# Kernel tuning notes

Measured on AMD Instinct MI355X. Metric: run time of the kernel, lower is better.

Reference implementation:

```python
import jax, jax.numpy as jnp
import numpy as np

# dims
B, N = 8, 64            # graphs, nodes per graph (equal-size ragged batch)
IN_DIM, EDGE_DIM = 16, 8
D, H = 128, 4
DH = D // H             # 32
L = 3                   # num_layers
FF = 4 * D              # 512
OUT = 1
SCALE = float(np.sqrt(DH))


def setup_inputs() -> dict:
    key = jax.random.key(0)
    ks = jax.random.split(key, 24)
    w = lambda k, s: jax.random.normal(k, s, jnp.float32) * 0.02
    return {
        'x': jax.random.normal(ks[0], (B, N, IN_DIM), jnp.float32),
        'edge_attr': jax.random.normal(ks[1], (B, N, N, EDGE_DIM), jnp.float32),
        'edge_mask': jax.random.bernoulli(ks[2], 0.2, (B, N, N)),
        # feature encoder (linear node + linear edge encoders, learned no-edge token)
        'node_W': w(ks[3], (IN_DIM, D)), 'node_b': jnp.zeros((D,), jnp.float32),
        'edge_W': w(ks[4], (EDGE_DIM, D)), 'edge_b': jnp.zeros((D,), jnp.float32),
        'no_edge': w(ks[5], (D,)),
        # per-layer edge-transformer params (stacked over L for lax.scan)
        'Wq': w(ks[6], (L, D, D)), 'Wk': w(ks[7], (L, D, D)),
        'Wv1': w(ks[8], (L, D, D)), 'Wv2': w(ks[9], (L, D, D)),
        'Wo': w(ks[10], (L, D, D)), 'bo': jnp.zeros((L, D), jnp.float32),
        'ln1_g': jnp.ones((L, D), jnp.float32), 'ln1_b': jnp.zeros((L, D), jnp.float32),
        'W1': w(ks[11], (L, D, FF)), 'b1': jnp.zeros((L, FF), jnp.float32),
        'W2': w(ks[12], (L, FF, D)), 'b2': jnp.zeros((L, D), jnp.float32),
        'ln2_g': jnp.ones((L, D), jnp.float32), 'ln2_b': jnp.zeros((L, D), jnp.float32),
        'Wout': w(ks[13], (D, OUT)), 'bout': jnp.zeros((OUT,), jnp.float32),
    }


def _ln(t, g, b):
    m = t.mean(-1, keepdims=True)
    v = t.var(-1, keepdims=True)
    return (t - m) * jax.lax.rsqrt(v + 1e-5) * g + b


def _forward(x, edge_attr, edge_mask, node_W, node_b, edge_W, edge_b, no_edge,
             Wq, Wk, Wv1, Wv2, Wo, bo, ln1_g, ln1_b, W1, b1, W2, b2,
             ln2_g, ln2_b, Wout, bout):
    # feature encoding: pair-token grid [B,N,N,D]
    node_emb = x @ node_W + node_b                       # [B,N,D]
    edge_emb = edge_attr @ edge_W + edge_b               # [B,N,N,D]
    tok = jnp.where(edge_mask[..., None], edge_emb, no_edge)
    eye = jnp.eye(N, dtype=bool)
    tok = jnp.where(eye[None, :, :, None], node_emb[:, :, None, :], tok)

    def heads(t, W):
        return (t @ W).reshape(B, N, N, H, DH)

    def layer(tok, p):
        wq, wk, wv1, wv2, wo, bo_, g1, b1_, w1, bf1, w2, bf2, g2, b2_ = p
        q = heads(tok, wq); k = heads(tok, wk)
        v1 = heads(tok, wv1); v2 = heads(tok, wv2)
        # triangular attention: token (i,j) attends over intermediate l
        s = jnp.einsum('bilhd,bljhd->bhilj', q, k) / SCALE   # [B,H,N,N,N]
        a = jax.nn.softmax(s, axis=3)                        # softmax over l
        o = jnp.einsum('bhilj,bilhd,bljhd->bijhd', a, v1, v2).reshape(B, N, N, D)
        tok = _ln(tok + o @ wo + bo_, g1, b1_)
        f = jax.nn.relu(tok @ w1 + bf1) @ w2 + bf2
        tok = _ln(tok + f, g2, b2_)
        return tok, None

    tok, _ = jax.lax.scan(
        layer, tok,
        (Wq, Wk, Wv1, Wv2, Wo, bo, ln1_g, ln1_b, W1, b1, W2, b2, ln2_g, ln2_b))

    diag = tok[:, jnp.arange(N), jnp.arange(N), :]           # node tokens [B,N,D]
    return diag @ Wout + bout                                 # [B,N,OUT]


def reference(x, edge_attr, edge_mask, node_W, node_b, edge_W, edge_b, no_edge,
              Wq, Wk, Wv1, Wv2, Wo, bo, ln1_g, ln1_b, W1, b1, W2, b2,
              ln2_g, ln2_b, Wout, bout):
    return _forward(x, edge_attr, edge_mask, node_W, node_b, edge_W, edge_b,
                    no_edge, Wq, Wk, Wv1, Wv2, Wo, bo, ln1_g, ln1_b,
                    W1, b1, W2, b2, ln2_g, ln2_b, Wout, bout)
```

## Files before the change

kernel.cpp:

```cpp
#include <hip/hip_runtime.h>

typedef unsigned short u16;
typedef __attribute__((ext_vector_type(8))) short bf16x8;
typedef __attribute__((ext_vector_type(4))) float f32x4;

#define INV_SCALE 0.17677669529663687f

static __device__ __forceinline__ float b2f(u16 u) {
    union { unsigned int i; float f; } v; v.i = ((unsigned int)u) << 16; return v.f;
}
static __device__ __forceinline__ u16 f2b(float f) {
    union { float f; unsigned int i; } v; v.f = f;
    unsigned int r = (v.i + 0x7FFFu + ((v.i >> 16) & 1u)) >> 16;
    return (u16)r;
}

#define NSEG 23
__device__ __constant__ int d_seg_off[NSEG + 1] = {
    0, 8192, 270336, 272384, 272512, 273536, 273664, 273792, 322944, 372096,
    421248, 470400, 519552, 519936, 520320, 520704, 717312, 718848, 915456,
    915840, 916224, 916608, 916736, 916744};
static const int h_seg_off[NSEG + 1] = {
    0, 8192, 270336, 272384, 272512, 273536, 273664, 273792, 322944, 372096,
    421248, 470400, 519552, 519936, 520320, 520704, 717312, 718848, 915456,
    915840, 916224, 916608, 916736, 916744};
#define ARENA_TOTAL 916744

struct ParamPtrs { const void* p[NSEG]; };

__global__ __launch_bounds__(256) void convert_params(ParamPtrs pp, u16* __restrict__ arena,
                                                      const void* __restrict__ mask,
                                                      int* __restrict__ mode) {
    if (blockIdx.x == 0) {
        __shared__ int f16, f32s, u8s;
        int tid = threadIdx.x;
        if (tid == 0) { f16 = 0; f32s = 0; u8s = 0; }
        __syncthreads();
        const u16* mu = (const u16*)mask;
        const unsigned int* mw = (const unsigned int*)mask;
        if (mu[2 * tid] == 0x3F80u) atomicOr(&f16, 1);
        if (mw[tid] == 0x3F800000u) atomicOr(&f32s, 1);
        if (mw[tid] > 1u) atomicOr(&u8s, 1);
        __syncthreads();
        if (tid == 0) mode[0] = f16 ? 0 : (f32s ? 3 : (u8s ? 1 : 2));
    }
    const unsigned int probe = ((const unsigned int*)pp.p[13])[0];
    const bool f32 = (probe == 0x3F800000u);
    for (int e = blockIdx.x * 256 + threadIdx.x; e < ARENA_TOTAL; e += gridDim.x * 256) {
        int k = 0;
        #pragma unroll
        for (int s2 = 1; s2 < NSEG; ++s2) if (e >= d_seg_off[s2]) k = s2;
        int local = e - d_seg_off[k];
        int src = local;
        if (k >= 7 && k <= 11) {
            int l = local >> 14, rem = local & 16383;
            int n = rem >> 7, kk = rem & 127;
            src = (l << 14) + kk * 128 + n;
        } else if (k == 15) {
            int l = local >> 16, rem = local & 65535;
            int n = rem >> 7, kk = rem & 127;
            src = (l << 16) + kk * 512 + n;
        } else if (k == 17) {
            int l = local >> 16, rem = local & 65535;
            int n = rem >> 9, kk = rem & 511;
            src = (l << 16) + kk * 128 + n;
        }
        u16 v;
        if (k == 22 && local >= 1) v = 0;
        else v = f32 ? f2b(((const float*)pp.p[k])[src]) : ((const u16*)pp.p[k])[src];
        arena[e] = v;
    }
}

__global__ __launch_bounds__(256) void assemble_kernel(
    const u16* __restrict__ x, const u16* __restrict__ ea,
    const void* __restrict__ mask, const int* __restrict__ modeptr,
    const u16* __restrict__ nodeW, const u16* __restrict__ nodeB,
    const u16* __restrict__ edgeW, const u16* __restrict__ edgeB, const u16* __restrict__ noedge,
    float* __restrict__ tokf, u16* __restrict__ tokb)
{
    const int md = modeptr[0];
    int g = blockIdx.x * 256 + threadIdx.x;
    int t = g >> 5, dq = g & 31, d0 = dq * 4;
    int b = t >> 12, i = (t >> 6) & 63, j = t & 63;
    float v[4];
    if (i == j) {
        #pragma unroll
        for (int c = 0; c < 4; c++) v[c] = b2f(nodeB[d0 + c]);
        #pragma unroll
        for (int e = 0; e < 16; e++) {
            float xe = b2f(x[(b * 64 + i) * 16 + e]);
            #pragma unroll
            for (int c = 0; c < 4; c++) v[c] += xe * b2f(nodeW[e * 128 + d0 + c]);
        }
    } else {
        bool edge;
        if (md == 0)      edge = ((const u16*)mask)[t] != 0;
        else if (md == 3) edge = ((const float*)mask)[t] != 0.0f;
        else if (md == 1) edge = ((const unsigned char*)mask)[t] != 0;
        else              edge = ((const unsigned int*)mask)[t] != 0;
        if (edge) {
            #pragma unroll
            for (int c = 0; c < 4; c++) v[c] = b2f(edgeB[d0 + c]);
            #pragma unroll
            for (int e = 0; e < 8; e++) {
                float ae = b2f(ea[t * 8 + e]);
                #pragma unroll
                for (int c = 0; c < 4; c++) v[c] += ae * b2f(edgeW[e * 128 + d0 + c]);
            }
        } else {
            #pragma unroll
            for (int c = 0; c < 4; c++) v[c] = b2f(noedge[d0 + c]);
        }
    }
    *(float4*)(tokf + (size_t)t * 128 + d0) = make_float4(v[0], v[1], v[2], v[3]);
    u16 pk[4];
    #pragma unroll
    for (int c = 0; c < 4; c++) pk[c] = f2b(v[c]);
    *(uint2*)(tokb + (size_t)t * 128 + d0) = *(uint2*)pk;
}

__global__ __launch_bounds__(256) void gemm_qkv_kernel(
    const u16* __restrict__ A,
    const u16* __restrict__ B0, const u16* __restrict__ B1,
    const u16* __restrict__ B2, const u16* __restrict__ B3,
    float* __restrict__ v1f,
    u16* __restrict__ qb, u16* __restrict__ kb, u16* __restrict__ v2b)
{
    __shared__ __align__(16) u16 smem[2 * 128 * 72];
    u16* As = smem;
    u16* Bs = smem + 128 * 72;
    int tid = threadIdx.x;
    int m0 = blockIdx.x * 128;
    int by = blockIdx.y;
    const u16* Bp = (by == 0) ? B0 : (by == 1) ? B1 : (by == 2) ? B2 : B3;

    int w = tid >> 6, lane = tid & 63;
    int q = lane >> 4, r16 = lane & 15;
    int rw = (w >> 1) * 64, cw = (w & 1) * 64;

    f32x4 acc[4][4];
    #pragma unroll
    for (int mi = 0; mi < 4; mi++)
        #pragma unroll
        for (int ni = 0; ni < 4; ni++) acc[mi][ni] = (f32x4){0.f, 0.f, 0.f, 0.f};

    #pragma unroll
    for (int kt = 0; kt < 2; ++kt) {
        int k0 = kt * 64;
        __syncthreads();
        #pragma unroll
        for (int it = 0; it < 4; ++it) {
            int idx = tid + it * 256;
            int row = idx >> 3, ch = idx & 7;
            uint4 d = *(const uint4*)(A + (size_t)(m0 + row) * 128 + k0 + ch * 8);
            *(uint4*)&As[row * 72 + ch * 8] = d;
        }
        #pragma unroll
        for (int it = 0; it < 4; ++it) {
            int idx = tid + it * 256;
            int n = idx >> 3, ch = idx & 7;
            uint4 d = *(const uint4*)(Bp + (size_t)n * 128 + k0 + ch * 8);
            int ch2 = ch ^ ((n >> 3) & 7);
            *(uint4*)&Bs[n * 72 + ch2 * 8] = d;
        }
        __syncthreads();
        #pragma unroll
        for (int ks = 0; ks < 2; ++ks) {
            bf16x8 fa[4], fb[4];
            #pragma unroll
            for (int mi = 0; mi < 4; mi++)
                fa[mi] = *(const bf16x8*)&As[(rw + mi * 16 + r16) * 72 + ks * 32 + q * 8];
            #pragma unroll
            for (int ni = 0; ni < 4; ni++) {
                int n = cw + ni * 16 + r16;
                int ch2 = (ks * 4 + q) ^ ((n >> 3) & 7);
                fb[ni] = *(const bf16x8*)&Bs[n * 72 + ch2 * 8];
            }
            #pragma unroll
            for (int mi = 0; mi < 4; mi++)
                #pragma unroll
                for (int ni = 0; ni < 4; ni++)
                    acc[mi][ni] = __builtin_amdgcn_mfma_f32_16x16x32_bf16(fa[mi], fb[ni], acc[mi][ni], 0, 0, 0);
        }
    }

    int bl = m0 >> 12, it0 = (m0 >> 6) & 63;
    __syncthreads();
    if (by == 2) {
        float* cf = (float*)smem;
        #pragma unroll
        for (int hp = 0; hp < 2; ++hp) {
            if (hp) __syncthreads();
            if ((cw >> 6) == hp) {
                #pragma unroll
                for (int mi = 0; mi < 4; mi++) {
                    #pragma unroll
                    for (int ni = 0; ni < 4; ni++) {
                        int colh = (cw & 63) + ni * 16 + r16;
                        int ch4 = colh >> 2, cl = colh & 3;
                        #pragma unroll
                        for (int rr = 0; rr < 4; rr++) {
                            int r = rw + mi * 16 + q * 4 + rr;
                            cf[r * 64 + (((ch4 ^ (r & 15)) << 2) | cl)] = acc[mi][ni][rr];
                        }
                    }
                }
            }
            __syncthreads();
            #pragma unroll
            for (int it = 0; it < 8; ++it) {
                int idx = tid + it * 256;
                int hh = idx >> 10, itl = (idx >> 9) & 1, jt = (idx >> 3) & 63, d4 = idx & 7;
                int r = itl * 64 + jt;
                int colh = hh * 32 + d4 * 4;
                f32x4 v = *(const f32x4*)&cf[r * 64 + (((colh >> 2) ^ (r & 15)) << 2)];
                int h = hp * 2 + hh;
                *(f32x4*)&v1f[((((size_t)(bl * 4 + h)) * 64 + it0 + itl) * 64 + jt) * 32 + d4 * 4] = v;
            }
        }
    } else {
        u16* cs = smem;
        #pragma unroll
        for (int mi = 0; mi < 4; mi++) {
            #pragma unroll
            for (int ni = 0; ni < 4; ni++) {
                int col = cw + ni * 16 + r16;
                int ch = col >> 3, cl = col & 7;
                #pragma unroll
                for (int rr = 0; rr < 4; rr++) {
                    int r = rw + mi * 16 + q * 4 + rr;
                    cs[r * 128 + (((ch ^ (r & 15)) << 3) | cl)] = f2b(acc[mi][ni][rr]);
                }
            }
        }
        __syncthreads();
        if (by == 0) {
            #pragma unroll
            for (int it = 0; it < 8; ++it) {
                int idx = tid + it * 256;
                int h = idx >> 9, jt = (idx >> 3) & 63, itl = (idx >> 2) & 1, d8 = idx & 3;
                int r = itl * 64 + jt, c8 = h * 4 + d8;
                uint4 d = *(const uint4*)&cs[r * 128 + ((c8 ^ (r & 15)) << 3)];
                *(uint4*)&qb[((((size_t)(bl * 4 + h)) * 64 + jt) * 64 + it0 + itl) * 32 + d8 * 8] = d;
            }
        } else {
            u16* dp = (by == 1) ? kb : v2b;
            #pragma unroll
            for (int it = 0; it < 8; ++it) {
                int idx = tid + it * 256;
                int h = idx >> 9, itl = (idx >> 8) & 1, jt = (idx >> 2) & 63, d8 = idx & 3;
                int r = itl * 64 + jt, c8 = h * 4 + d8;
                uint4 d = *(const uint4*)&cs[r * 128 + ((c8 ^ (r & 15)) << 3)];
                *(uint4*)&dp[((((size_t)(bl * 4 + h)) * 64 + it0 + itl) * 64 + jt) * 32 + d8 * 8] = d;
            }
        }
    }
}

__global__ __launch_bounds__(256) void gemm_ln_kernel(
    const u16* __restrict__ A,
    const u16* __restrict__ BT,
    const u16* __restrict__ bias,
    float* __restrict__ tokf,
    const u16* __restrict__ lng, const u16* __restrict__ lnb, u16* __restrict__ tokbO)
{
    __shared__ __align__(16) u16 smem[64 * 72 + 128 * 72];
    u16* As = smem;
    u16* Bs = smem + 64 * 72;
    int tid = threadIdx.x;
    int m0 = blockIdx.x * 64;
    int w = tid >> 6, lane = tid & 63;
    int q = lane >> 4, r16 = lane & 15;
    int rw = (w >> 1) * 32, cw = (w & 1) * 64;

    f32x4 acc[2][4];
    #pragma unroll
    for (int mi = 0; mi < 2; mi++)
        #pragma unroll
        for (int ni = 0; ni < 4; ni++) acc[mi][ni] = (f32x4){0.f, 0.f, 0.f, 0.f};

    #pragma unroll
    for (int kt = 0; kt < 2; ++kt) {
        int k0 = kt * 64;
        __syncthreads();
        #pragma unroll
        for (int it = 0; it < 2; ++it) {
            int idx = tid + it * 256;
            int row = idx >> 3, ch = idx & 7;
            uint4 d = *(const uint4*)(A + (size_t)(m0 + row) * 128 + k0 + ch * 8);
            *(uint4*)&As[row * 72 + ch * 8] = d;
        }
        #pragma unroll
        for (int it = 0; it < 4; ++it) {
            int idx = tid + it * 256;
            int n = idx >> 3, ch = idx & 7;
            uint4 d = *(const uint4*)(BT + (size_t)n * 128 + k0 + ch * 8);
            int ch2 = ch ^ ((n >> 3) & 7);
            *(uint4*)&Bs[n * 72 + ch2 * 8] = d;
        }
        __syncthreads();
        #pragma unroll
        for (int ks = 0; ks < 2; ++ks) {
            bf16x8 fa[2], fb[4];
            #pragma unroll
            for (int mi = 0; mi < 2; mi++)
                fa[mi] = *(const bf16x8*)&As[(rw + mi * 16 + r16) * 72 + ks * 32 + q * 8];
            #pragma unroll
            for (int ni = 0; ni < 4; ni++) {
                int n = cw + ni * 16 + r16;
                int ch2 = (ks * 4 + q) ^ ((n >> 3) & 7);
                fb[ni] = *(const bf16x8*)&Bs[n * 72 + ch2 * 8];
            }
            #pragma unroll
            for (int mi = 0; mi < 2; mi++)
                #pragma unroll
                for (int ni = 0; ni < 4; ni++)
                    acc[mi][ni] = __builtin_amdgcn_mfma_f32_16x16x32_bf16(fa[mi], fb[ni], acc[mi][ni], 0, 0, 0);
        }
    }

    __syncthreads();
    float* cf  = (float*)smem;
    float* rsm = cf + 64 * 64;
    float* rqm = rsm + 128;
    int half = cw >> 6;
    #pragma unroll
    for (int ni = 0; ni < 4; ni++) {
        int col = cw + ni * 16 + r16;
        float bb = b2f(bias[col]);
        #pragma unroll
        for (int mi = 0; mi < 2; mi++)
            #pragma unroll
            for (int rr = 0; rr < 4; rr++) {
                int r = rw + mi * 16 + q * 4 + rr;
                acc[mi][ni][rr] += bb + tokf[(size_t)(m0 + r) * 128 + col];
            }
    }
    #pragma unroll
    for (int mi = 0; mi < 2; mi++)
        #pragma unroll
        for (int rr = 0; rr < 4; rr++) {
            float s = 0.f, sq = 0.f;
            #pragma unroll
            for (int ni = 0; ni < 4; ni++) { float t = acc[mi][ni][rr]; s += t; sq += t * t; }
            #pragma unroll
            for (int off = 1; off < 16; off <<= 1) {
                s  += __shfl_xor(s,  off, 16);
                sq += __shfl_xor(sq, off, 16);
            }
            if (r16 == 0) {
                int r = rw + mi * 16 + q * 4 + rr;
                rsm[half * 64 + r] = s;
                rqm[half * 64 + r] = sq;
            }
        }
    __syncthreads();
    float gl[4], bv[4];
    #pragma unroll
    for (int ni = 0; ni < 4; ni++) {
        int col = cw + ni * 16 + r16;
        gl[ni] = b2f(lng[col]);
        bv[ni] = b2f(lnb[col]);
    }
    #pragma unroll
    for (int mi = 0; mi < 2; mi++)
        #pragma unroll
        for (int rr = 0; rr < 4; rr++) {
            int r = rw + mi * 16 + q * 4 + rr;
            float tot = rsm[r] + rsm[64 + r];
            float tq  = rqm[r] + rqm[64 + r];
            float mean = tot * 0.0078125f;
            float var  = tq * 0.0078125f - mean * mean;
            float rstd = rsqrtf(var + 1e-5f);
            #pragma unroll
            for (int ni = 0; ni < 4; ni++)
                acc[mi][ni][rr] = (acc[mi][ni][rr] - mean) * rstd * gl[ni] + bv[ni];
        }
    #pragma unroll
    for (int hp = 0; hp < 2; ++hp) {
        __syncthreads();
        if (half == hp) {
            #pragma unroll
            for (int mi = 0; mi < 2; mi++)
                #pragma unroll
                for (int ni = 0; ni < 4; ni++) {
                    int colh = (cw & 63) + ni * 16 + r16;
                    int ch4 = colh >> 2, cl = colh & 3;
                    #pragma unroll
                    for (int rr = 0; rr < 4; rr++) {
                        int r = rw + mi * 16 + q * 4 + rr;
                        cf[r * 64 + (((ch4 ^ (r & 15)) << 2) | cl)] = acc[mi][ni][rr];
                    }
                }
        }
        __syncthreads();
        #pragma unroll
        for (int it = 0; it < 4; ++it) {
            int idx = tid + it * 256;
            int r = idx >> 4, c4 = idx & 15;
            f32x4 v = *(const f32x4*)&cf[r * 64 + ((c4 ^ (r & 15)) << 2)];
            int col = hp * 64 + c4 * 4;
            *(f32x4*)(tokf + (size_t)(m0 + r) * 128 + col) = v;
            u16 pk[4];
            #pragma unroll
            for (int e = 0; e < 4; e++) pk[e] = f2b(v[e]);
            *(uint2*)(tokbO + (size_t)(m0 + r) * 128 + col) = *(uint2*)pk;
        }
    }
}

__global__ __launch_bounds__(256) void ff_kernel(
    const u16* __restrict__ A,
    const u16* __restrict__ W1T, const u16* __restrict__ b1,
    const u16* __restrict__ W2T, const u16* __restrict__ b2,
    const u16* __restrict__ lng, const u16* __restrict__ lnb,
    float* __restrict__ tokf, u16* __restrict__ tokbO)
{
    __shared__ __align__(16) u16 smem[64 * 72 + 128 * 72];
    u16* As = smem;
    u16* Bs = smem + 64 * 72;
    int tid = threadIdx.x;
    int m0 = blockIdx.x * 64;
    int w = tid >> 6, lane = tid & 63;
    int q = lane >> 4, r16 = lane & 15;
    int rw = (w >> 1) * 32, cw = (w & 1) * 64;

    f32x4 acc2[2][4];
    #pragma unroll
    for (int mi = 0; mi < 2; mi++)
        #pragma unroll
        for (int ni = 0; ni < 4; ni++) acc2[mi][ni] = (f32x4){0.f, 0.f, 0.f, 0.f};

    for (int hs = 0; hs < 4; ++hs) {
        f32x4 acc1[2][4];
        #pragma unroll
        for (int mi = 0; mi < 2; mi++)
            #pragma unroll
            for (int ni = 0; ni < 4; ni++) acc1[mi][ni] = (f32x4){0.f, 0.f, 0.f, 0.f};
        #pragma unroll
        for (int kt = 0; kt < 2; ++kt) {
            int k0 = kt * 64;
            __syncthreads();
            #pragma unroll
            for (int it = 0; it < 2; ++it) {
                int idx = tid + it * 256;
                int row = idx >> 3, ch = idx & 7;
                uint4 d = *(const uint4*)(A + (size_t)(m0 + row) * 128 + k0 + ch * 8);
                *(uint4*)&As[row * 72 + ch * 8] = d;
            }
            #pragma unroll
            for (int it = 0; it < 4; ++it) {
                int idx = tid + it * 256;
                int n = idx >> 3, ch = idx & 7;
                uint4 d = *(const uint4*)(W1T + (size_t)(hs * 128 + n) * 128 + k0 + ch * 8);
                int ch2 = ch ^ ((n >> 3) & 7);
                *(uint4*)&Bs[n * 72 + ch2 * 8] = d;
            }
            __syncthreads();
            #pragma unroll
            for (int ks = 0; ks < 2; ++ks) {
                bf16x8 fa[2], fb[4];
                #pragma unroll
                for (int mi = 0; mi < 2; mi++)
                    fa[mi] = *(const bf16x8*)&As[(rw + mi * 16 + r16) * 72 + ks * 32 + q * 8];
                #pragma unroll
                for (int ni = 0; ni < 4; ni++) {
                    int n = cw + ni * 16 + r16;
                    int ch2 = (ks * 4 + q) ^ ((n >> 3) & 7);
                    fb[ni] = *(const bf16x8*)&Bs[n * 72 + ch2 * 8];
                }
                #pragma unroll
                for (int mi = 0; mi < 2; mi++)
                    #pragma unroll
                    for (int ni = 0; ni < 4; ni++)
                        acc1[mi][ni] = __builtin_amdgcn_mfma_f32_16x16x32_bf16(fa[mi], fb[ni], acc1[mi][ni], 0, 0, 0);
            }
        }
        #pragma unroll
        for (int half = 0; half < 2; ++half) {
            __syncthreads();
            if ((w & 1) == half) {
                #pragma unroll
                for (int mi = 0; mi < 2; mi++)
                    #pragma unroll
                    for (int ni = 0; ni < 4; ni++) {
                        int kl = ni * 16 + r16;
                        float bb = b2f(b1[hs * 128 + half * 64 + kl]);
                        #pragma unroll
                        for (int rr = 0; rr < 4; rr++) {
                            int row = rw + mi * 16 + q * 4 + rr;
                            As[row * 72 + kl] = f2b(fmaxf(acc1[mi][ni][rr] + bb, 0.f));
                        }
                    }
            }
            #pragma unroll
            for (int it = 0; it < 4; ++it) {
                int idx = tid + it * 256;
                int n = idx >> 3, ch = idx & 7;
                uint4 d = *(const uint4*)(W2T + (size_t)n * 512 + hs * 128 + half * 64 + ch * 8);
                int ch2 = ch ^ ((n >> 3) & 7);
                *(uint4*)&Bs[n * 72 + ch2 * 8] = d;
            }
            __syncthreads();
            #pragma unroll
            for (int ks = 0; ks < 2; ++ks) {
                bf16x8 fa[2], fb[4];
                #pragma unroll
                for (int mi = 0; mi < 2; mi++)
                    fa[mi] = *(const bf16x8*)&As[(rw + mi * 16 + r16) * 72 + ks * 32 + q * 8];
                #pragma unroll
                for (int ni = 0; ni < 4; ni++) {
                    int n = cw + ni * 16 + r16;
                    int ch2 = (ks * 4 + q) ^ ((n >> 3) & 7);
                    fb[ni] = *(const bf16x8*)&Bs[n * 72 + ch2 * 8];
                }
                #pragma unroll
                for (int mi = 0; mi < 2; mi++)
                    #pragma unroll
                    for (int ni = 0; ni < 4; ni++)
                        acc2[mi][ni] = __builtin_amdgcn_mfma_f32_16x16x32_bf16(fa[mi], fb[ni], acc2[mi][ni], 0, 0, 0);
            }
        }
    }

    __syncthreads();
    float* cf  = (float*)smem;
    float* rsm = cf + 64 * 64;
    float* rqm = rsm + 128;
    int half = cw >> 6;
    #pragma unroll
    for (int ni = 0; ni < 4; ni++) {
        int col = cw + ni * 16 + r16;
        float bb = b2f(b2[col]);
        #pragma unroll
        for (int mi = 0; mi < 2; mi++)
            #pragma unroll
            for (int rr = 0; rr < 4; rr++) {
                int r = rw + mi * 16 + q * 4 + rr;
                acc2[mi][ni][rr] += bb + tokf[(size_t)(m0 + r) * 128 + col];
            }
    }
    #pragma unroll
    for (int mi = 0; mi < 2; mi++)
        #pragma unroll
        for (int rr = 0; rr < 4; rr++) {
            float s = 0.f, sq = 0.f;
            #pragma unroll
            for (int ni = 0; ni < 4; ni++) { float t = acc2[mi][ni][rr]; s += t; sq += t * t; }
            #pragma unroll
            for (int off = 1; off < 16; off <<= 1) {
                s  += __shfl_xor(s,  off, 16);
                sq += __shfl_xor(sq, off, 16);
            }
            if (r16 == 0) {
                int r = rw + mi * 16 + q * 4 + rr;
                rsm[half * 64 + r] = s;
                rqm[half * 64 + r] = sq;
            }
        }
    __syncthreads();
    float gl[4], bv[4];
    #pragma unroll
    for (int ni = 0; ni < 4; ni++) {
        int col = cw + ni * 16 + r16;
        gl[ni] = b2f(lng[col]);
        bv[ni] = b2f(lnb[col]);
    }
    #pragma unroll
    for (int mi = 0; mi < 2; mi++)
        #pragma unroll
        for (int rr = 0; rr < 4; rr++) {
            int r = rw + mi * 16 + q * 4 + rr;
            float tot = rsm[r] + rsm[64 + r];
            float tq  = rqm[r] + rqm[64 + r];
            float mean = tot * 0.0078125f;
            float var  = tq * 0.0078125f - mean * mean;
            float rstd = rsqrtf(var + 1e-5f);
            #pragma unroll
            for (int ni = 0; ni < 4; ni++)
                acc2[mi][ni][rr] = (acc2[mi][ni][rr] - mean) * rstd * gl[ni] + bv[ni];
        }
    #pragma unroll
    for (int hp = 0; hp < 2; ++hp) {
        __syncthreads();
        if (half == hp) {
            #pragma unroll
            for (int mi = 0; mi < 2; mi++)
                #pragma unroll
                for (int ni = 0; ni < 4; ni++) {
                    int colh = (cw & 63) + ni * 16 + r16;
                    int ch4 = colh >> 2, cl = colh & 3;
                    #pragma unroll
                    for (int rr = 0; rr < 4; rr++) {
                        int r = rw + mi * 16 + q * 4 + rr;
                        cf[r * 64 + (((ch4 ^ (r & 15)) << 2) | cl)] = acc2[mi][ni][rr];
                    }
                }
        }
        __syncthreads();
        #pragma unroll
        for (int it = 0; it < 4; ++it) {
            int idx = tid + it * 256;
            int r = idx >> 4, c4 = idx & 15;
            f32x4 v = *(const f32x4*)&cf[r * 64 + ((c4 ^ (r & 15)) << 2)];
            int col = hp * 64 + c4 * 4;
            *(f32x4*)(tokf + (size_t)(m0 + r) * 128 + col) = v;
            u16 pk[4];
            #pragma unroll
            for (int e = 0; e < 4; e++) pk[e] = f2b(v[e]);
            *(uint2*)(tokbO + (size_t)(m0 + r) * 128 + col) = *(uint2*)pk;
        }
    }
}

__global__ __launch_bounds__(64) void attn_s_kernel(
    const u16* __restrict__ qb, const u16* __restrict__ kb, u16* __restrict__ s)
{
    __shared__ __align__(16) u16 sm[64 * 80];
    u16* qs  = sm;
    u16* ks_ = sm + 64 * 40;
    int g = blockIdx.x;
    int l = g & 63, bh = g >> 6;
    const u16* Q = qb + ((size_t)bh * 64 + l) * 2048;
    const u16* Kp = kb + ((size_t)bh * 64 + l) * 2048;
    int lane = threadIdx.x;
    #pragma unroll
    for (int it = 0; it < 4; ++it) {
        int idx = lane + it * 64;
        int row = idx >> 2, c4 = idx & 3;
        *(uint4*)&qs[row * 40 + c4 * 8] = *(const uint4*)(Q + row * 32 + c4 * 8);
        *(uint4*)&ks_[row * 40 + c4 * 8] = *(const uint4*)(Kp + row * 32 + c4 * 8);
    }
    __syncthreads();
    int q = lane >> 4, r16 = lane & 15;
    f32x4 acc[4][4];
    #pragma unroll
    for (int mi = 0; mi < 4; mi++)
        #pragma unroll
        for (int ni = 0; ni < 4; ni++) acc[mi][ni] = (f32x4){0.f, 0.f, 0.f, 0.f};
    bf16x8 fa[4], fb[4];
    #pragma unroll
    for (int mi = 0; mi < 4; mi++) fa[mi] = *(const bf16x8*)&qs[(mi * 16 + r16) * 40 + q * 8];
    #pragma unroll
    for (int ni = 0; ni < 4; ni++) fb[ni] = *(const bf16x8*)&ks_[(ni * 16 + r16) * 40 + q * 8];
    #pragma unroll
    for (int mi = 0; mi < 4; mi++)
        #pragma unroll
        for (int ni = 0; ni < 4; ni++)
            acc[mi][ni] = __builtin_amdgcn_mfma_f32_16x16x32_bf16(fa[mi], fb[ni], acc[mi][ni], 0, 0, 0);
    __syncthreads();
    u16* cs = sm;
    #pragma unroll
    for (int mi = 0; mi < 4; mi++)
        #pragma unroll
        for (int ni = 0; ni < 4; ni++)
            #pragma unroll
            for (int rr = 0; rr < 4; rr++)
                cs[(mi * 16 + q * 4 + rr) * 72 + ni * 16 + r16] = f2b(acc[mi][ni][rr] * INV_SCALE);
    __syncthreads();
    u16* sb = s + (size_t)bh * 262144 + l * 64;
    #pragma unroll
    for (int it = 0; it < 8; ++it) {
        int row = it * 8 + (lane >> 3);
        uint4 d = *(const uint4*)&cs[row * 72 + (lane & 7) * 8];
        *(uint4*)&sb[(size_t)row * 4096 + (lane & 7) * 8] = d;
    }
}

__global__ __launch_bounds__(256) void attn_o_kernel(
    const u16* __restrict__ a, const float* __restrict__ v1f, const u16* __restrict__ v2b,
    u16* __restrict__ ob)
{
    __shared__ __align__(16) float v2s[4 * 1152];
    __shared__ __align__(16) u16   as_[8 * 4 * 32];
    __shared__ __align__(16) float v1s[8 * 4 * 32];
    int bh = blockIdx.x;
    int i0 = blockIdx.y * 8;
    int jh = blockIdx.z;
    int bl = bh >> 2, h = bh & 3;
    int tid = threadIdx.x;
    int j32 = tid & 31;
    int ih = (tid >> 5) & 1;
    int dh = (tid >> 6) * 8;
    int jg = jh * 32 + j32;
    const u16*   v2base = v2b + (size_t)bh * 131072;
    const float* v1base = v1f + (size_t)bh * 131072 + (size_t)i0 * 2048;
    const u16*   abase  = a + (size_t)bh * 262144 + (size_t)i0 * 4096;

    int lz[2], jz[2], cz[2];
    #pragma unroll
    for (int it = 0; it < 2; ++it) {
        int idx = tid + it * 256;
        lz[it] = idx >> 7; jz[it] = (idx >> 2) & 31; cz[it] = idx & 3;
    }
    int ia = tid >> 5, la = (tid >> 3) & 3, jaq = tid & 7;
    int iv = tid >> 5, lv = (tid >> 3) & 3, dvq = (tid & 7) * 4;

    uint4 pv2[2]; uint2 pa; f32x4 pv1;

#define LOAD_CHUNK(l0_)                                                             \
    _Pragma("unroll")                                                               \
    for (int it = 0; it < 2; ++it)                                                  \
        pv2[it] = *(const uint4*)(v2base + ((size_t)((l0_) + lz[it]) * 64 + jh * 32 + jz[it]) * 32 + cz[it] * 8); \
    pa  = *(const uint2*)(abase + (size_t)ia * 4096 + ((l0_) + la) * 64 + jh * 32 + jaq * 4); \
    pv1 = *(const f32x4*)(v1base + (size_t)iv * 2048 + ((l0_) + lv) * 32 + dvq);

#define STORE_CHUNK()                                                               \
    _Pragma("unroll")                                                               \
    for (int it = 0; it < 2; ++it) {                                                \
        const u16* ds = (const u16*)&pv2[it];                                       \
        float* dst = &v2s[lz[it] * 1152 + jz[it] * 36 + cz[it] * 8];                \
        _Pragma("unroll")                                                           \
        for (int e = 0; e < 8; e++) dst[e] = b2f(ds[e]);                            \
    }                                                                               \
    *(uint2*)&as_[ia * 128 + la * 32 + jaq * 4] = pa;                               \
    *(f32x4*)&v1s[iv * 128 + lv * 32 + dvq] = pv1;

    float acc[4][8];
    float Z[4];
    #pragma unroll
    for (int i = 0; i < 4; i++) {
        Z[i] = 0.f;
        #pragma unroll
        for (int e = 0; e < 8; e++) acc[i][e] = 0.f;
    }

    LOAD_CHUNK(0);
    for (int ch = 0; ch < 16; ++ch) {
        if (ch) __syncthreads();
        STORE_CHUNK();
        if (ch + 1 < 16) LOAD_CHUNK((ch + 1) * 4);
        __syncthreads();
        #pragma unroll
        for (int lc = 0; lc < 4; ++lc) {
            const float* vp = &v2s[lc * 1152 + j32 * 36 + dh];
            float v2r[8];
            *(f32x4*)&v2r[0] = *(const f32x4*)vp;
            *(f32x4*)&v2r[4] = *(const f32x4*)(vp + 4);
            #pragma unroll
            for (int ii = 0; ii < 4; ++ii) {
                int iL = ih * 4 + ii;
                float sv = b2f(as_[iL * 128 + lc * 32 + j32]);
                float av = __expf(sv);
                Z[ii] += av;
                const float* v1p = &v1s[iL * 128 + lc * 32 + dh];
                #pragma unroll
                for (int e = 0; e < 8; e++)
                    acc[ii][e] += (av * v1p[e]) * v2r[e];
            }
        }
    }
#undef LOAD_CHUNK
#undef STORE_CHUNK

    #pragma unroll
    for (int ii = 0; ii < 4; ++ii) {
        int iL = ih * 4 + ii;
        float sc = 1.0f / Z[ii];
        u16 tmp[8];
        #pragma unroll
        for (int e = 0; e < 8; e++) tmp[e] = f2b(acc[ii][e] * sc);
        *(uint4*)(ob + ((size_t)(bl * 64 + i0 + iL) * 64 + jg) * 128 + h * 32 + dh) = *(uint4*)tmp;
    }
}

__global__ __launch_bounds__(256) void out_kernel(
    const float* __restrict__ tokf, const u16* __restrict__ Wout, const u16* __restrict__ bout,
    float* __restrict__ out)
{
    int g = blockIdx.x * 256 + threadIdx.x;
    int b = g >> 6, i = g & 63;
    const float* p = tokf + ((size_t)(b * 64 + i) * 64 + i) * 128;
    float s = b2f(bout[0]);
    #pragma unroll
    for (int d = 0; d < 128; d++) s += p[d] * b2f(Wout[d]);
    out[g] = s;
}

extern "C" void kernel_launch(void* const* d_in, const int* in_sizes, int n_in,
                              void* d_out, int out_size, void* d_ws, size_t ws_size,
                              hipStream_t stream) {
    const void* mask = d_in[2];
    ParamPtrs pp;
    for (int k = 0; k < NSEG; ++k) pp.p[k] = d_in[k < 2 ? k : k + 1];

    char* ws = (char*)d_ws;
    u16* arena = (u16*)ws;
    #define AP(k) ((const u16*)ws + h_seg_off[k])
    int*   mmode = (int*)(ws + 1835008);
    float* tokf  = (float*)(ws + 2097152);
    u16*   tokb  = (u16*)(ws + 18874368);
    const size_t base = 27262976;
    const size_t MB = 1048576ULL;

    int NB = 8;
    while (NB > 1 && base + (size_t)NB * 7 * MB > ws_size) NB >>= 1;

    u16*   qb  = (u16*)(ws + base);
    u16*   kb  = (u16*)(ws + base + (size_t)NB * MB);
    u16*   v2b = (u16*)(ws + base + (size_t)NB * 2 * MB);
    float* v1f = (float*)(ws + base + (size_t)NB * 3 * MB);
    u16*   sb  = (u16*)(ws + base + (size_t)NB * 5 * MB);
    u16*   ob  = qb;

    convert_params<<<1024, 256, 0, stream>>>(pp, arena, mask, mmode);
    assemble_kernel<<<4096, 256, 0, stream>>>(AP(0), AP(1), mask, mmode,
                                              AP(2), AP(3), AP(4), AP(5), AP(6), tokf, tokb);

    for (int l = 0; l < 3; ++l) {
        const u16* Wq_l  = AP(7)  + l * 16384;
        const u16* Wk_l  = AP(8)  + l * 16384;
        const u16* Wv1_l = AP(9)  + l * 16384;
        const u16* Wv2_l = AP(10) + l * 16384;
        const u16* Wo_l  = AP(11) + l * 16384;
        const u16* bo_l  = AP(12) + l * 128;
        const u16* g1_l  = AP(13) + l * 128;
        const u16* be1_l = AP(14) + l * 128;
        const u16* W1_l  = AP(15) + l * 65536;
        const u16* b1_l  = AP(16) + l * 512;
        const u16* W2_l  = AP(17) + l * 65536;
        const u16* b2_l  = AP(18) + l * 128;
        const u16* g2_l  = AP(19) + l * 128;
        const u16* be2_l = AP(20) + l * 128;

        for (int r = 0; r < 8 / NB; ++r) {
            size_t rowOff = (size_t)r * NB * 4096;
            gemm_qkv_kernel<<<dim3(NB * 32, 4), 256, 0, stream>>>(
                tokb + rowOff * 128, Wq_l, Wk_l, Wv1_l, Wv2_l,
                v1f, qb, kb, v2b);
            attn_s_kernel<<<NB * 256, 64, 0, stream>>>(qb, kb, sb);
            attn_o_kernel<<<dim3(NB * 4, 8, 2), 256, 0, stream>>>(sb, v1f, v2b, ob);
            gemm_ln_kernel<<<NB * 64, 256, 0, stream>>>(
                ob, Wo_l, bo_l, tokf + rowOff * 128,
                g1_l, be1_l, tokb + rowOff * 128);
        }
        ff_kernel<<<512, 256, 0, stream>>>(tokb, W1_l, b1_l, W2_l, b2_l,
                                           g2_l, be2_l, tokf, tokb);
    }
    out_kernel<<<2, 256, 0, stream>>>(tokf, AP(21), AP(22), (float*)d_out);
}
```

Measured before the change: 413.9 us.

## Fuse output projection, LN1 and feed-forward block into one kernel with register prefetch

Merges the Wo projection with LayerNorm1 and the FF MLP with LayerNorm2 into a single kernel per row tile. The normalized LN1 output stays in shared memory as bf16 and its fp32 residual stays in registers, so there is no global write and re-read of tokf/tokb between the two stages and one launch per layer goes away. It also adds software prefetch of the next weight and activation tile into registers, overlapping global loads with the MFMA loop. The costs are higher register pressure and more shared memory per block (about 46KB), which can lower occupancy, and FF now runs inside the NB chunk loop instead of as one 512-block launch.

```diff
diff --git a/kernel.cpp b/kernel.cpp
--- a/kernel.cpp
+++ b/kernel.cpp
@@ -258,21 +258,66 @@
     }
 }
 
-__global__ __launch_bounds__(256) void gemm_ln_kernel(
+__global__ __launch_bounds__(256) void fuse2_kernel(
     const u16* __restrict__ A,
-    const u16* __restrict__ BT,
-    const u16* __restrict__ bias,
-    float* __restrict__ tokf,
-    const u16* __restrict__ lng, const u16* __restrict__ lnb, u16* __restrict__ tokbO)
+    const u16* __restrict__ WoT, const u16* __restrict__ bo,
+    const u16* __restrict__ g1, const u16* __restrict__ be1,
+    const u16* __restrict__ W1T, const u16* __restrict__ b1,
+    const u16* __restrict__ W2T, const u16* __restrict__ b2,
+    const u16* __restrict__ g2, const u16* __restrict__ be2,
+    float* __restrict__ tokf, u16* __restrict__ tokbO)
 {
-    __shared__ __align__(16) u16 smem[64 * 72 + 128 * 72];
+    __shared__ __align__(16) u16 smem[9216 + 9216 + 4608];
     u16* As = smem;
-    u16* Bs = smem + 64 * 72;
+    u16* Bs = smem + 9216;
+    u16* Hs = smem + 18432;
     int tid = threadIdx.x;
     int m0 = blockIdx.x * 64;
     int w = tid >> 6, lane = tid & 63;
     int q = lane >> 4, r16 = lane & 15;
     int rw = (w >> 1) * 32, cw = (w & 1) * 64;
+    int half_w = cw >> 6;
+
+    int bn[4], bch[4], bch2[4];
+    #pragma unroll
+    for (int it = 0; it < 4; ++it) {
+        int idx = tid + it * 256;
+        bn[it] = idx >> 3; bch[it] = idx & 7;
+        bch2[it] = bch[it] ^ ((bn[it] >> 3) & 7);
+    }
+    int an[2], ach[2];
+    #pragma unroll
+    for (int it = 0; it < 2; ++it) {
+        int idx = tid + it * 256;
+        an[it] = idx >> 3; ach[it] = idx & 7;
+    }
+
+    uint4 pb[4], pa[2];
+
+#define LDB(ptr_, ldr_, roff_, coff_)                                               \
+    do {                                                                            \
+        _Pragma("unroll")                                                           \
+        for (int it = 0; it < 4; ++it)                                              \
+            pb[it] = *(const uint4*)((ptr_) + (size_t)((roff_) + bn[it]) * (ldr_) + (coff_) + bch[it] * 8); \
+    } while (0)
+#define STB()                                                                       \
+    do {                                                                            \
+        _Pragma("unroll")                                                           \
+        for (int it = 0; it < 4; ++it)                                              \
+            *(uint4*)&Bs[bn[it] * 72 + bch2[it] * 8] = pb[it];                      \
+    } while (0)
+#define LDA(kt_)                                                                    \
+    do {                                                                            \
+        _Pragma("unroll")                                                           \
+        for (int it = 0; it < 2; ++it)                                              \
+            pa[it] = *(const uint4*)(A + (size_t)(m0 + an[it]) * 128 + (kt_) * 64 + ach[it] * 8); \
+    } while (0)
+#define STA()                                                                       \
+    do {                                                                            \
+        _Pragma("unroll")                                                           \
+        for (int it = 0; it < 2; ++it)                                              \
+            *(uint4*)&Hs[an[it] * 72 + ach[it] * 8] = pa[it];                       \
+    } while (0)
 
     f32x4 acc[2][4];
     #pragma unroll
@@ -280,32 +325,20 @@
         #pragma unroll
         for (int ni = 0; ni < 4; ni++) acc[mi][ni] = (f32x4){0.f, 0.f, 0.f, 0.f};
 
+    LDA(0); LDB(WoT, 128, 0, 0);
     #pragma unroll
     for (int kt = 0; kt < 2; ++kt) {
-        int k0 = kt * 64;
-        __syncthreads();
-        #pragma unroll
-        for (int it = 0; it < 2; ++it) {
-            int idx = tid + it * 256;
-            int row = idx >> 3, ch = idx & 7;
-            uint4 d = *(const uint4*)(A + (size_t)(m0 + row) * 128 + k0 + ch * 8);
-            *(uint4*)&As[row * 72 + ch * 8] = d;
-        }
-        #pragma unroll
-        for (int it = 0; it < 4; ++it) {
-            int idx = tid + it * 256;
-            int n = idx >> 3, ch = idx & 7;
-            uint4 d = *(const uint4*)(BT + (size_t)n * 128 + k0 + ch * 8);
-            int ch2 = ch ^ ((n >> 3) & 7);
-            *(uint4*)&Bs[n * 72 + ch2 * 8] = d;
-        }
+        if (kt) __syncthreads();
+        STA(); STB();
+        if (kt == 0) { LDA(1); LDB(WoT, 128, 0, 64); }
+        else         { LDB(W1T, 128, 0, 0); }
         __syncthreads();
         #pragma unroll
         for (int ks = 0; ks < 2; ++ks) {
             bf16x8 fa[2], fb[4];
             #pragma unroll
             for (int mi = 0; mi < 2; mi++)
-                fa[mi] = *(const bf16x8*)&As[(rw + mi * 16 + r16) * 72 + ks * 32 + q * 8];
+                fa[mi] = *(const bf16x8*)&Hs[(rw + mi * 16 + r16) * 72 + ks * 32 + q * 8];
             #pragma unroll
             for (int ni = 0; ni < 4; ni++) {
                 int n = cw + ni * 16 + r16;
@@ -320,15 +353,10 @@
         }
     }
 
-    __syncthreads();
-    float* cf  = (float*)smem;
-    float* rsm = cf + 64 * 64;
-    float* rqm = rsm + 128;
-    int half = cw >> 6;
     #pragma unroll
     for (int ni = 0; ni < 4; ni++) {
         int col = cw + ni * 16 + r16;
-        float bb = b2f(bias[col]);
+        float bb = b2f(bo[col]);
         #pragma unroll
         for (int mi = 0; mi < 2; mi++)
             #pragma unroll
@@ -337,94 +365,63 @@
                 acc[mi][ni][rr] += bb + tokf[(size_t)(m0 + r) * 128 + col];
             }
     }
-    #pragma unroll
-    for (int mi = 0; mi < 2; mi++)
-        #pragma unroll
-        for (int rr = 0; rr < 4; rr++) {
-            float s = 0.f, sq = 0.f;
-            #pragma unroll
-            for (int ni = 0; ni < 4; ni++) { float t = acc[mi][ni][rr]; s += t; sq += t * t; }
-            #pragma unroll
-            for (int off = 1; off < 16; off <<= 1) {
-                s  += __shfl_xor(s,  off, 16);
-                sq += __shfl_xor(sq, off, 16);
-            }
-            if (r16 == 0) {
+    __syncthreads();
+    {
+        float* rsm = (float*)Hs;
+        float* rqm = rsm + 128;
+        #pragma unroll
+        for (int mi = 0; mi < 2; mi++)
+            #pragma unroll
+            for (int rr = 0; rr < 4; rr++) {
+                float s = 0.f, sq = 0.f;
+                #pragma unroll
+                for (int ni = 0; ni < 4; ni++) { float t = acc[mi][ni][rr]; s += t; sq += t * t; }
+                #pragma unroll
+                for (int off = 1; off < 16; off <<= 1) {
+                    s  += __shfl_xor(s,  off, 16);
+                    sq += __shfl_xor(sq, off, 16);
+                }
+                if (r16 == 0) {
+                    int r = rw + mi * 16 + q * 4 + rr;
+                    rsm[half_w * 64 + r] = s;
+                    rqm[half_w * 64 + r] = sq;
+                }
+            }
+        __syncthreads();
+        float gl[4], bv[4];
+        #pragma unroll
+        for (int ni = 0; ni < 4; ni++) {
+            int col = cw + ni * 16 + r16;
+            gl[ni] = b2f(g1[col]);
+            bv[ni] = b2f(be1[col]);
+        }
+        #pragma unroll
+        for (int mi = 0; mi < 2; mi++)
+            #pragma unroll
+            for (int rr = 0; rr < 4; rr++) {
                 int r = rw + mi * 16 + q * 4 + rr;
-                rsm[half * 64 + r] = s;
-                rqm[half * 64 + r] = sq;
-            }
-        }
+                float tot = rsm[r] + rsm[64 + r];
+                float tq  = rqm[r] + rqm[64 + r];
+                float mean = tot * 0.0078125f;
+                float var  = tq * 0.0078125f - mean * mean;
+                float rstd = rsqrtf(var + 1e-5f);
+                #pragma unroll
+                for (int ni = 0; ni < 4; ni++)
+                    acc[mi][ni][rr] = (acc[mi][ni][rr] - mean) * rstd * gl[ni] + bv[ni];
+            }
+        #pragma unroll
+        for (int mi = 0; mi < 2; mi++)
+            #pragma unroll
+            for (int ni = 0; ni < 4; ni++) {
+                int cl = ni * 16 + r16;
+                #pragma unroll
+                for (int rr = 0; rr < 4; rr++) {
+                    int r = rw + mi * 16 + q * 4 + rr;
+                    As[half_w * 4608 + r * 72 + cl] = f2b(acc[mi][ni][rr]);
+                }
+            }
+    }
     __syncthreads();
-    float gl[4], bv[4];
-    #pragma unroll
-    for (int ni = 0; ni < 4; ni++) {
-        int col = cw + ni * 16 + r16;
-        gl[ni] = b2f(lng[col]);
-        bv[ni] = b2f(lnb[col]);
-    }
-    #pragma unroll
-    for (int mi = 0; mi < 2; mi++)
-        #pragma unroll
-        for (int rr = 0; rr < 4; rr++) {
-            int r = rw + mi * 16 + q * 4 + rr;
-            float tot = rsm[r] + rsm[64 + r];
-            float tq  = rqm[r] + rqm[64 + r];
-            float mean = tot * 0.0078125f;
-            float var  = tq * 0.0078125f - mean * mean;
-            float rstd = rsqrtf(var + 1e-5f);
-            #pragma unroll
-            for (int ni = 0; ni < 4; ni++)
-                acc[mi][ni][rr] = (acc[mi][ni][rr] - mean) * rstd * gl[ni] + bv[ni];
-        }
-    #pragma unroll
-    for (int hp = 0; hp < 2; ++hp) {
-        __syncthreads();
-        if (half == hp) {
-            #pragma unroll
-            for (int mi = 0; mi < 2; mi++)
-                #pragma unroll
-                for (int ni = 0; ni < 4; ni++) {
-                    int colh = (cw & 63) + ni * 16 + r16;
-                    int ch4 = colh >> 2, cl = colh & 3;
-                    #pragma unroll
-                    for (int rr = 0; rr < 4; rr++) {
-                        int r = rw + mi * 16 + q * 4 + rr;
-                        cf[r * 64 + (((ch4 ^ (r & 15)) << 2) | cl)] = acc[mi][ni][rr];
-                    }
-                }
-        }
-        __syncthreads();
-        #pragma unroll
-        for (int it = 0; it < 4; ++it) {
-            int idx = tid + it * 256;
-            int r = idx >> 4, c4 = idx & 15;
-            f32x4 v = *(const f32x4*)&cf[r * 64 + ((c4 ^ (r & 15)) << 2)];
-            int col = hp * 64 + c4 * 4;
-            *(f32x4*)(tokf + (size_t)(m0 + r) * 128 + col) = v;
-            u16 pk[4];
-            #pragma unroll
-            for (int e = 0; e < 4; e++) pk[e] = f2b(v[e]);
-            *(uint2*)(tokbO + (size_t)(m0 + r) * 128 + col) = *(uint2*)pk;
-        }
-    }
-}
-
-__global__ __launch_bounds__(256) void ff_kernel(
-    const u16* __restrict__ A,
-    const u16* __restrict__ W1T, const u16* __restrict__ b1,
-    const u16* __restrict__ W2T, const u16* __restrict__ b2,
-    const u16* __restrict__ lng, const u16* __restrict__ lnb,
-    float* __restrict__ tokf, u16* __restrict__ tokbO)
-{
-    __shared__ __align__(16) u16 smem[64 * 72 + 128 * 72];
-    u16* As = smem;
-    u16* Bs = smem + 64 * 72;
-    int tid = threadIdx.x;
-    int m0 = blockIdx.x * 64;
-    int w = tid >> 6, lane = tid & 63;
-    int q = lane >> 4, r16 = lane & 15;
-    int rw = (w >> 1) * 32, cw = (w & 1) * 64;
 
     f32x4 acc2[2][4];
     #pragma unroll
@@ -440,30 +437,17 @@
             for (int ni = 0; ni < 4; ni++) acc1[mi][ni] = (f32x4){0.f, 0.f, 0.f, 0.f};
         #pragma unroll
         for (int kt = 0; kt < 2; ++kt) {
-            int k0 = kt * 64;
-            __syncthreads();
-            #pragma unroll
-            for (int it = 0; it < 2; ++it) {
-                int idx = tid + it * 256;
-                int row = idx >> 3, ch = idx & 7;
-                uint4 d = *(const uint4*)(A + (size_t)(m0 + row) * 128 + k0 + ch * 8);
-                *(uint4*)&As[row * 72 + ch * 8] = d;
-            }
-            #pragma unroll
-            for (int it = 0; it < 4; ++it) {
-                int idx = tid + it * 256;
-                int n = idx >> 3, ch = idx & 7;
-                uint4 d = *(const uint4*)(W1T + (size_t)(hs * 128 + n) * 128 + k0 + ch * 8);
-                int ch2 = ch ^ ((n >> 3) & 7);
-                *(uint4*)&Bs[n * 72 + ch2 * 8] = d;
-            }
+            if (hs || kt) __syncthreads();
+            STB();
+            if (kt == 0) { LDB(W1T, 128, hs * 128, 64); }
+            else         { LDB(W2T, 512, 0, hs * 128); }
             __syncthreads();
             #pragma unroll
             for (int ks = 0; ks < 2; ++ks) {
                 bf16x8 fa[2], fb[4];
                 #pragma unroll
                 for (int mi = 0; mi < 2; mi++)
-                    fa[mi] = *(const bf16x8*)&As[(rw + mi * 16 + r16) * 72 + ks * 32 + q * 8];
+                    fa[mi] = *(const bf16x8*)&As[kt * 4608 + (rw + mi * 16 + r16) * 72 + ks * 32 + q * 8];
                 #pragma unroll
                 for (int ni = 0; ni < 4; ni++) {
                     int n = cw + ni * 16 + r16;
@@ -490,25 +474,20 @@
                         #pragma unroll
                         for (int rr = 0; rr < 4; rr++) {
                             int row = rw + mi * 16 + q * 4 + rr;
-                            As[row * 72 + kl] = f2b(fmaxf(acc1[mi][ni][rr] + bb, 0.f));
+                            Hs[row * 72 + kl] = f2b(fmaxf(acc1[mi][ni][rr] + bb, 0.f));
                         }
                     }
             }
-            #pragma unroll
-            for (int it = 0; it < 4; ++it) {
-                int idx = tid + it * 256;
-                int n = idx >> 3, ch = idx & 7;
-                uint4 d = *(const uint4*)(W2T + (size_t)n * 512 + hs * 128 + half * 64 + ch * 8);
-                int ch2 = ch ^ ((n >> 3) & 7);
-                *(uint4*)&Bs[n * 72 + ch2 * 8] = d;
-            }
+            STB();
+            if (half == 0)   { LDB(W2T, 512, 0, hs * 128 + 64); }
+            else if (hs < 3) { LDB(W1T, 128, (hs + 1) * 128, 0); }
             __syncthreads();
             #pragma unroll
             for (int ks = 0; ks < 2; ++ks) {
                 bf16x8 fa[2], fb[4];
                 #pragma unroll
                 for (int mi = 0; mi < 2; mi++)
-                    fa[mi] = *(const bf16x8*)&As[(rw + mi * 16 + r16) * 72 + ks * 32 + q * 8];
+                    fa[mi] = *(const bf16x8*)&Hs[(rw + mi * 16 + r16) * 72 + ks * 32 + q * 8];
                 #pragma unroll
                 for (int ni = 0; ni < 4; ni++) {
                     int n = cw + ni * 16 + r16;
@@ -525,10 +504,9 @@
     }
 
     __syncthreads();
-    float* cf  = (float*)smem;
-    float* rsm = cf + 64 * 64;
-    float* rqm = rsm + 128;
-    int half = cw >> 6;
+    float* cf   = (float*)smem;
+    float* rsm2 = cf + 64 * 64;
+    float* rqm2 = rsm2 + 128;
     #pragma unroll
     for (int ni = 0; ni < 4; ni++) {
         int col = cw + ni * 16 + r16;
@@ -536,10 +514,8 @@
         #pragma unroll
         for (int mi = 0; mi < 2; mi++)
             #pragma unroll
-            for (int rr = 0; rr < 4; rr++) {
-                int r = rw + mi * 16 + q * 4 + rr;
-                acc2[mi][ni][rr] += bb + tokf[(size_t)(m0 + r) * 128 + col];
-            }
+            for (int rr = 0; rr < 4; rr++)
+                acc2[mi][ni][rr] += bb + acc[mi][ni][rr];
     }
     #pragma unroll
     for (int mi = 0; mi < 2; mi++)
@@ -555,36 +531,38 @@
             }
             if (r16 == 0) {
                 int r = rw + mi * 16 + q * 4 + rr;
-                rsm[half * 64 + r] = s;
-                rqm[half * 64 + r] = sq;
+                rsm2[half_w * 64 + r] = s;
+                rqm2[half_w * 64 + r] = sq;
             }
         }
     __syncthreads();
-    float gl[4], bv[4];
-    #pragma unroll
-    for (int ni = 0; ni < 4; ni++) {
-        int col = cw + ni * 16 + r16;
-        gl[ni] = b2f(lng[col]);
-        bv[ni] = b2f(lnb[col]);
-    }
-    #pragma unroll
-    for (int mi = 0; mi < 2; mi++)
-        #pragma unroll
-        for (int rr = 0; rr < 4; rr++) {
-            int r = rw + mi * 16 + q * 4 + rr;
-            float tot = rsm[r] + rsm[64 + r];
-            float tq  = rqm[r] + rqm[64 + r];
-            float mean = tot * 0.0078125f;
-            float var  = tq * 0.0078125f - mean * mean;
-            float rstd = rsqrtf(var + 1e-5f);
-            #pragma unroll
-            for (int ni = 0; ni < 4; ni++)
-                acc2[mi][ni][rr] = (acc2[mi][ni][rr] - mean) * rstd * gl[ni] + bv[ni];
-        }
+    {
+        float gl[4], bv[4];
+        #pragma unroll
+        for (int ni = 0; ni < 4; ni++) {
+            int col = cw + ni * 16 + r16;
+            gl[ni] = b2f(g2[col]);
+            bv[ni] = b2f(be2[col]);
+        }
+        #pragma unroll
+        for (int mi = 0; mi < 2; mi++)
+            #pragma unroll
+            for (int rr = 0; rr < 4; rr++) {
+                int r = rw + mi * 16 + q * 4 + rr;
+                float tot = rsm2[r] + rsm2[64 + r];
+                float tq  = rqm2[r] + rqm2[64 + r];
+                float mean = tot * 0.0078125f;
+                float var  = tq * 0.0078125f - mean * mean;
+                float rstd = rsqrtf(var + 1e-5f);
+                #pragma unroll
+                for (int ni = 0; ni < 4; ni++)
+                    acc2[mi][ni][rr] = (acc2[mi][ni][rr] - mean) * rstd * gl[ni] + bv[ni];
+            }
+    }
     #pragma unroll
     for (int hp = 0; hp < 2; ++hp) {
         __syncthreads();
-        if (half == hp) {
+        if (half_w == hp) {
             #pragma unroll
             for (int mi = 0; mi < 2; mi++)
                 #pragma unroll
@@ -612,6 +590,10 @@
             *(uint2*)(tokbO + (size_t)(m0 + r) * 128 + col) = *(uint2*)pk;
         }
     }
+#undef LDB
+#undef STB
+#undef LDA
+#undef STA
 }
 
 __global__ __launch_bounds__(64) void attn_s_kernel(
@@ -831,12 +813,10 @@
                 v1f, qb, kb, v2b);
             attn_s_kernel<<<NB * 256, 64, 0, stream>>>(qb, kb, sb);
             attn_o_kernel<<<dim3(NB * 4, 8, 2), 256, 0, stream>>>(sb, v1f, v2b, ob);
-            gemm_ln_kernel<<<NB * 64, 256, 0, stream>>>(
-                ob, Wo_l, bo_l, tokf + rowOff * 128,
-                g1_l, be1_l, tokb + rowOff * 128);
-        }
-        ff_kernel<<<512, 256, 0, stream>>>(tokb, W1_l, b1_l, W2_l, b2_l,
-                                           g2_l, be2_l, tokf, tokb);
+            fuse2_kernel<<<NB * 64, 256, 0, stream>>>(
+                ob, Wo_l, bo_l, g1_l, be1_l, W1_l, b1_l, W2_l, b2_l, g2_l, be2_l,
+                tokf + rowOff * 128, tokb + rowOff * 128);
+        }
     }
     out_kernel<<<2, 256, 0, stream>>>(tokf, AP(21), AP(22), (float*)d_out);
 }
```

Measured after the change: 491.0 us. 18.6% more time.
